# Optimization experiments

Hardware: AMD Instinct MI355X
Metric: run time of the kernel (lower is better)

The kernel has to match this reference:

```python
import jax, jax.numpy as jnp
import numpy as np

NUM_GRAPHS = 64
NUM_LAYERS = 3
HEADS = 4
HID = 64
DMODEL = HEADS * HID  # 256
NUM_EDGE_TYPES = 8
NUM_CLASSES = 2
N_NODES = 30000
N_EDGES = 240000


def setup_inputs() -> dict:
    key = jax.random.key(0)
    ks = jax.random.split(key, 16)
    s = 0.05
    x = jax.random.normal(ks[0], (N_NODES, DMODEL), jnp.float32)
    edge_index = jax.random.randint(ks[1], (2, N_EDGES), 0, N_NODES)
    batch = jnp.sort(jax.random.randint(ks[2], (N_NODES,), 0, NUM_GRAPHS))
    edge_type_ids = jax.random.randint(ks[3], (N_EDGES,), 0, NUM_EDGE_TYPES)
    # stacked per-layer conv params (all layers are DMODEL -> HEADS*HID = DMODEL)
    Wq = jax.random.normal(ks[4], (NUM_LAYERS, DMODEL, DMODEL), jnp.float32) * s
    bq = jax.random.normal(ks[5], (NUM_LAYERS, DMODEL), jnp.float32) * s
    Wk = jax.random.normal(ks[6], (NUM_LAYERS, DMODEL, DMODEL), jnp.float32) * s
    bk = jax.random.normal(ks[7], (NUM_LAYERS, DMODEL), jnp.float32) * s
    Wv = jax.random.normal(ks[8], (NUM_LAYERS, DMODEL, DMODEL), jnp.float32) * s
    bv = jax.random.normal(ks[9], (NUM_LAYERS, DMODEL), jnp.float32) * s
    Eemb = jax.random.normal(ks[10], (NUM_LAYERS, NUM_EDGE_TYPES, DMODEL), jnp.float32) * s
    # 1-layer GRU (PyTorch layout: [3*hid, in], gate order r, z, n)
    W_ih = jax.random.normal(ks[11], (3 * HID, DMODEL), jnp.float32) * s
    b_ih = jax.random.normal(ks[12], (3 * HID,), jnp.float32) * s
    W_hh = jax.random.normal(ks[13], (3 * HID, HID), jnp.float32) * s
    b_hh = jax.random.normal(ks[14], (3 * HID,), jnp.float32) * s
    W_fc = jax.random.normal(ks[15], (NUM_CLASSES, HID), jnp.float32) * s
    b_fc = jnp.zeros((NUM_CLASSES,), jnp.float32)
    return dict(x=x, edge_index=edge_index, batch=batch, edge_type_ids=edge_type_ids,
                Wq=Wq, bq=bq, Wk=Wk, bk=bk, Wv=Wv, bv=bv, Eemb=Eemb,
                W_ih=W_ih, b_ih=b_ih, W_hh=W_hh, b_hh=b_hh, W_fc=W_fc, b_fc=b_fc)


def reference(x, edge_index, batch, edge_type_ids, Wq, bq, Wk, bk, Wv, bv, Eemb,
              W_ih, b_ih, W_hh, b_hh, W_fc, b_fc):
    N = x.shape[0]
    src, dst = edge_index[0], edge_index[1]  # messages flow src -> dst
    scale = 1.0 / jnp.sqrt(jnp.float32(HID))
    for l in range(NUM_LAYERS):
        q = (x @ Wq[l] + bq[l]).reshape(N, HEADS, HID)
        k_all = x @ Wk[l] + bk[l]  # [N, DMODEL]
        v_all = x @ Wv[l] + bv[l]
        ete = Eemb[l][edge_type_ids]  # edge-type conditioning, [E, DMODEL]
        k = (k_all[src] + ete).reshape(-1, HEADS, HID)
        v = (v_all[src] + ete).reshape(-1, HEADS, HID)
        scores = jnp.einsum('ehd,ehd->eh', q[dst], k) * scale  # [E, H]
        # per-destination-node segment softmax (stable)
        m = jax.ops.segment_max(scores, dst, num_segments=N)
        ex = jnp.exp(scores - m[dst])
        den = jax.ops.segment_sum(ex, dst, num_segments=N)
        alpha = ex / (den[dst] + 1e-16)
        agg = jax.ops.segment_sum(alpha[..., None] * v, dst, num_segments=N)
        x = jax.nn.elu(agg.reshape(N, DMODEL))
    # global mean pool over graphs
    cnt = jax.ops.segment_sum(jnp.ones((N,), x.dtype), batch, num_segments=NUM_GRAPHS)
    g = jax.ops.segment_sum(x, batch, num_segments=NUM_GRAPHS) / jnp.maximum(cnt, 1.0)[:, None]
    # single GRU step from h0 = 0 (seq_len == 1)
    h0 = jnp.zeros((NUM_GRAPHS, HID), x.dtype)
    gi = g @ W_ih.T + b_ih
    gh = h0 @ W_hh.T + b_hh
    ir, iz, inn = jnp.split(gi, 3, axis=-1)
    hr, hz, hn = jnp.split(gh, 3, axis=-1)
    r = jax.nn.sigmoid(ir + hr)
    z = jax.nn.sigmoid(iz + hz)
    n = jnp.tanh(inn + r * hn)
    h = (1.0 - z) * n + z * h0
    return h @ W_fc.T + b_fc  # [NUM_GRAPHS, NUM_CLASSES]
```

## Files before the change

kernel.cpp:

```cpp
#include <hip/hip_runtime.h>
#include <math.h>

#define N_NODES 30000
#define N_EDGES 240000
#define DMODEL 256
#define NETYPES 8
#define NGRAPHS 64
#define NLAYERS 3

typedef __attribute__((ext_vector_type(8))) short short8;
typedef __attribute__((ext_vector_type(4))) float f32x4;

__device__ __forceinline__ unsigned short f2bf(float f) {
  union { float f; unsigned u; } v; v.f = f;
  unsigned r = v.u + 0x7FFF + ((v.u >> 16) & 1);
  return (unsigned short)(r >> 16);
}
__device__ __forceinline__ float bf2f(unsigned short h) {
  union { unsigned u; float f; } v; v.u = ((unsigned)h) << 16;
  return v.f;
}

__device__ __forceinline__ void async_g2l(const unsigned short* g, unsigned short* l) {
  __builtin_amdgcn_global_load_lds(
      (const __attribute__((address_space(1))) void*)g,
      (__attribute__((address_space(3))) void*)l, 16, 0, 0);
}

__device__ __forceinline__ float dpp_red_add(float x) {
  int v = __float_as_int(x);
  int t;
  t = __builtin_amdgcn_update_dpp(0, v, 0xB1, 0xF, 0xF, true);
  v = __float_as_int(__int_as_float(v) + __int_as_float(t));
  t = __builtin_amdgcn_update_dpp(0, v, 0x4E, 0xF, 0xF, true);
  v = __float_as_int(__int_as_float(v) + __int_as_float(t));
  t = __builtin_amdgcn_update_dpp(0, v, 0x141, 0xF, 0xF, true);
  v = __float_as_int(__int_as_float(v) + __int_as_float(t));
  t = __builtin_amdgcn_update_dpp(0, v, 0x140, 0xF, 0xF, true);
  v = __float_as_int(__int_as_float(v) + __int_as_float(t));
  return __int_as_float(v);
}

__global__ void k_count_deg(const int* __restrict__ dst, int* __restrict__ deg) {
  int e = blockIdx.x * blockDim.x + threadIdx.x;
  if (e < N_EDGES) atomicAdd(&deg[dst[e]], 1);
}

__global__ __launch_bounds__(1024) void k_scan(const int* __restrict__ deg,
                                               int* __restrict__ rowstart,
                                               int* __restrict__ cursor) {
  const int C = 30;
  int tid = threadIdx.x;
  int base = tid * C;
  int vals[C];
  int sum = 0;
#pragma unroll
  for (int j = 0; j < C; ++j) {
    int idx = base + j;
    int v = (idx < N_NODES) ? deg[idx] : 0;
    vals[j] = sum;
    sum += v;
  }
  int lane = tid & 63, wv = tid >> 6;
  int s = sum;
#pragma unroll
  for (int off = 1; off < 64; off <<= 1) {
    int t2 = __shfl_up(s, off);
    if (lane >= off) s += t2;
  }
  __shared__ int wsum[16];
  if (lane == 63) wsum[wv] = s;
  __syncthreads();
  if (tid == 0) {
    int a = 0;
#pragma unroll
    for (int i = 0; i < 16; ++i) { int t2 = wsum[i]; wsum[i] = a; a += t2; }
    rowstart[N_NODES] = a;
  }
  __syncthreads();
  int texcl = wsum[wv] + (s - sum);
#pragma unroll
  for (int j = 0; j < C; ++j) {
    int idx = base + j;
    if (idx < N_NODES) {
      int p = texcl + vals[j];
      rowstart[idx] = p;
      cursor[idx]   = p;
    }
  }
}

__global__ void k_scatter(const int* __restrict__ src, const int* __restrict__ dst,
                          const int* __restrict__ etype, int* __restrict__ cursor,
                          int* __restrict__ packed) {
  int e = blockIdx.x * blockDim.x + threadIdx.x;
  if (e < N_EDGES) {
    int p = atomicAdd(&cursor[dst[e]], 1);
    packed[p] = src[e] * NETYPES + etype[e];
  }
}

__global__ __launch_bounds__(256) void k_cvt_w(
    const float* __restrict__ Wq, const float* __restrict__ Wk, const float* __restrict__ Wv,
    unsigned short* __restrict__ wthi) {
  __shared__ float tile[32][33];
  int k0 = blockIdx.x * 32;
  int n0g = blockIdx.y * 32;
  int l = blockIdx.z;
  int which = n0g >> 8;
  int col0 = n0g & 255;
  const float* W = (which == 0) ? Wq : ((which == 1) ? Wk : Wv);
  int c = threadIdx.x & 31, r = threadIdx.x >> 5;
#pragma unroll
  for (int rr = 0; rr < 4; ++rr) {
    int kk = r + rr * 8;
    tile[kk][c] = W[(size_t)l * 65536 + (size_t)(k0 + kk) * 256 + col0 + c];
  }
  __syncthreads();
  int kk = threadIdx.x & 31, nn0 = threadIdx.x >> 5;
#pragma unroll
  for (int rr = 0; rr < 4; ++rr) {
    int nn = nn0 + rr * 8;
    wthi[((size_t)l * 768 + n0g + nn) * 256 + k0 + kk] = f2bf(tile[kk][nn]);
  }
}

__global__ void k_cvt_b(const float* __restrict__ bq, const float* __restrict__ bk,
                        const float* __restrict__ bv, float* __restrict__ bcat) {
  int idx = blockIdx.x * 256 + threadIdx.x;
  if (idx >= NLAYERS * 768) return;
  int n = idx % 768, l = idx / 768;
  int which = n >> 8, col = n & 255;
  const float* b = (which == 0) ? bq : ((which == 1) ? bk : bv);
  bcat[idx] = b[l * 256 + col];
}

__global__ void k_cvt_x(const float* __restrict__ x, unsigned short* __restrict__ xhi,
                        unsigned short* __restrict__ xlo) {
  int i = blockIdx.x * 256 + threadIdx.x;
  if (i < N_NODES * 256) {
    float v = x[i];
    unsigned short h = f2bf(v);
    xhi[i] = h;
    xlo[i] = f2bf(v - bf2f(h));
  }
}

__global__ __launch_bounds__(256) void k_gemm_mfma(
    const unsigned short* __restrict__ Ahi, const unsigned short* __restrict__ Alo,
    const unsigned short* __restrict__ Bhi,
    const float* __restrict__ bcat, float* __restrict__ qbuf,
    unsigned short* __restrict__ kv) {
  __shared__ unsigned short smem[2 * 12288];

  int tid = threadIdx.x;
  int lane = tid & 63, wave = tid >> 6;
  int bx = blockIdx.x;
  int xcd = bx & 7, slot = bx >> 3;
  int rt = xcd + (slot / 6) * 8;
  if (rt >= 235) return;
  int row0 = rt * 128;
  int n0 = (slot % 6) * 128;
  int wm = (wave >> 1) * 64, wn = (wave & 1) * 64;
  int quad = lane >> 4, l16 = lane & 15;
  int chunk = lane & 3;
  int srow = wave * 32 + (lane >> 2);

  f32x4 acc[4][4];
#pragma unroll
  for (int i = 0; i < 4; ++i)
#pragma unroll
    for (int j = 0; j < 4; ++j) acc[i][j] = (f32x4)(0.f);

  auto STAGE = [&](int k0, int b) {
    unsigned short* s = smem + b * 12288;
#pragma unroll
    for (int j = 0; j < 2; ++j) {
      int r = srow + j * 16;
      int ldsoff = wave * 1024 + j * 512;
      int garA = row0 + r; if (garA >= N_NODES) garA = N_NODES - 1;
      size_t aoff = (size_t)garA * 256 + k0 + chunk * 8;
      async_g2l(Ahi + aoff, s + ldsoff);
      async_g2l(Alo + aoff, s + 4096 + ldsoff);
      size_t boff = (size_t)(n0 + r) * 256 + k0 + chunk * 8;
      async_g2l(Bhi + boff, s + 8192 + ldsoff);
    }
  };

  STAGE(0, 0);
#pragma unroll
  for (int k = 0; k < 8; ++k) {
    int cur = k & 1;
    if (k < 7) {
      STAGE((k + 1) * 32, cur ^ 1);
      asm volatile("s_waitcnt vmcnt(6)" ::: "memory");
    } else {
      asm volatile("s_waitcnt vmcnt(0)" ::: "memory");
    }
    __builtin_amdgcn_s_barrier();

    const unsigned short* sAhi = smem + cur * 12288;
    const unsigned short* sAlo = sAhi + 4096;
    const unsigned short* sBhi = sAhi + 8192;
    short8 ah[4], al[4], bh[4];
#pragma unroll
    for (int i = 0; i < 4; ++i) {
      int off = (wm + i * 16 + l16) * 32 + quad * 8;
      ah[i] = *(const short8*)(sAhi + off);
      al[i] = *(const short8*)(sAlo + off);
    }
#pragma unroll
    for (int j = 0; j < 4; ++j) {
      int off = (wn + j * 16 + l16) * 32 + quad * 8;
      bh[j] = *(const short8*)(sBhi + off);
    }
#pragma unroll
    for (int i = 0; i < 4; ++i)
#pragma unroll
      for (int j = 0; j < 4; ++j) {
        acc[i][j] = __builtin_amdgcn_mfma_f32_16x16x32_bf16(ah[i], bh[j], acc[i][j], 0, 0, 0);
        acc[i][j] = __builtin_amdgcn_mfma_f32_16x16x32_bf16(al[i], bh[j], acc[i][j], 0, 0, 0);
      }
    __builtin_amdgcn_s_barrier();
  }

  float bj[4];
#pragma unroll
  for (int j = 0; j < 4; ++j) bj[j] = bcat[n0 + wn + j * 16 + l16];
  bool isq = (n0 < 256);
#pragma unroll
  for (int i = 0; i < 4; ++i) {
    int rowb = row0 + wm + i * 16 + quad * 4;
#pragma unroll
    for (int r = 0; r < 4; ++r) {
      int grow = rowb + r;
      if (grow < N_NODES) {
        if (isq) {
          float* cp = qbuf + (size_t)grow * 256 + n0 + wn + l16;
#pragma unroll
          for (int j = 0; j < 4; ++j) cp[j * 16] = acc[i][j][r] + bj[j];
        } else {
          unsigned short* cp = kv + (size_t)grow * 512 + (n0 - 256) + wn + l16;
#pragma unroll
          for (int j = 0; j < 4; ++j) cp[j * 16] = f2bf(acc[i][j][r] + bj[j]);
        }
      }
    }
  }
}

__global__ __launch_bounds__(256) void k_attn(
    const float* __restrict__ qbuf, const unsigned short* __restrict__ kv,
    const int* __restrict__ rowstart, const int* __restrict__ packed,
    const float* __restrict__ Eemb_l,
    unsigned short* __restrict__ xhi, unsigned short* __restrict__ xlo) {
  __shared__ float ete_s[NETYPES * 256];
  int t = threadIdx.x;
#pragma unroll
  for (int i = 0; i < NETYPES; ++i) ete_s[i * 256 + t] = Eemb_l[i * 256 + t];
  __syncthreads();
  int lane = t & 63;
  int n = blockIdx.x * 4 + (t >> 6);
  float4 q4 = ((const float4*)(qbuf + (size_t)n * 256))[lane];
  int rs = rowstart[n], re = rowstart[n + 1];
  float l1 = 0.f, ax1 = 0.f, ay1 = 0.f, az1 = 0.f, aw1 = 0.f;
  float l2 = 0.f, ax2 = 0.f, ay2 = 0.f, az2 = 0.f, aw2 = 0.f;
  int i = rs;
  for (; i + 2 <= re; i += 2) {
    int pkA = packed[i], pkB = packed[i + 1];
    const unsigned short* baseA = kv + (size_t)(pkA >> 3) * 512;
    const unsigned short* baseB = kv + (size_t)(pkB >> 3) * 512;
    ushort4 kA = ((const ushort4*)baseA)[lane];
    ushort4 vA = ((const ushort4*)(baseA + 256))[lane];
    ushort4 kB = ((const ushort4*)baseB)[lane];
    ushort4 vB = ((const ushort4*)(baseB + 256))[lane];
    float4 eA = ((const float4*)(ete_s + (pkA & 7) * 256))[lane];
    float4 eB = ((const float4*)(ete_s + (pkB & 7) * 256))[lane];
    float pA = (bf2f(kA.x) + eA.x) * q4.x + (bf2f(kA.y) + eA.y) * q4.y +
               (bf2f(kA.z) + eA.z) * q4.z + (bf2f(kA.w) + eA.w) * q4.w;
    float pB = (bf2f(kB.x) + eB.x) * q4.x + (bf2f(kB.y) + eB.y) * q4.y +
               (bf2f(kB.z) + eB.z) * q4.z + (bf2f(kB.w) + eB.w) * q4.w;
    pA = dpp_red_add(pA);
    pB = dpp_red_add(pB);
    float e1 = __expf(pA * 0.125f);
    float e2 = __expf(pB * 0.125f);
    l1 += e1; l2 += e2;
    ax1 = fmaf(e1, bf2f(vA.x) + eA.x, ax1);
    ay1 = fmaf(e1, bf2f(vA.y) + eA.y, ay1);
    az1 = fmaf(e1, bf2f(vA.z) + eA.z, az1);
    aw1 = fmaf(e1, bf2f(vA.w) + eA.w, aw1);
    ax2 = fmaf(e2, bf2f(vB.x) + eB.x, ax2);
    ay2 = fmaf(e2, bf2f(vB.y) + eB.y, ay2);
    az2 = fmaf(e2, bf2f(vB.z) + eB.z, az2);
    aw2 = fmaf(e2, bf2f(vB.w) + eB.w, aw2);
  }
  if (i < re) {
    int pk = packed[i];
    const unsigned short* base = kv + (size_t)(pk >> 3) * 512;
    ushort4 kh = ((const ushort4*)base)[lane];
    ushort4 vh = ((const ushort4*)(base + 256))[lane];
    float4 e4 = ((const float4*)(ete_s + (pk & 7) * 256))[lane];
    float p = (bf2f(kh.x) + e4.x) * q4.x + (bf2f(kh.y) + e4.y) * q4.y +
              (bf2f(kh.z) + e4.z) * q4.z + (bf2f(kh.w) + e4.w) * q4.w;
    p = dpp_red_add(p);
    float e1 = __expf(p * 0.125f);
    l1 += e1;
    ax1 = fmaf(e1, bf2f(vh.x) + e4.x, ax1);
    ay1 = fmaf(e1, bf2f(vh.y) + e4.y, ay1);
    az1 = fmaf(e1, bf2f(vh.z) + e4.z, az1);
    aw1 = fmaf(e1, bf2f(vh.w) + e4.w, aw1);
  }
  float l = l1 + l2;
  float inv = 1.f / (l + 1e-16f);
  float4 o;
  o.x = (ax1 + ax2) * inv; o.y = (ay1 + ay2) * inv;
  o.z = (az1 + az2) * inv; o.w = (aw1 + aw2) * inv;
  o.x = o.x > 0.f ? o.x : expm1f(o.x);
  o.y = o.y > 0.f ? o.y : expm1f(o.y);
  o.z = o.z > 0.f ? o.z : expm1f(o.z);
  o.w = o.w > 0.f ? o.w : expm1f(o.w);
  unsigned short h0 = f2bf(o.x), h1 = f2bf(o.y), h2 = f2bf(o.z), h3 = f2bf(o.w);
  ushort4 hv, lv;
  hv.x = h0; hv.y = h1; hv.z = h2; hv.w = h3;
  lv.x = f2bf(o.x - bf2f(h0)); lv.y = f2bf(o.y - bf2f(h1));
  lv.z = f2bf(o.z - bf2f(h2)); lv.w = f2bf(o.w - bf2f(h3));
  size_t base_o = (size_t)n * 256 + lane * 4;
  *(ushort4*)(xhi + base_o) = hv;
  *(ushort4*)(xlo + base_o) = lv;
}

__global__ __launch_bounds__(256) void k_pool_partial(
    const unsigned short* __restrict__ xhi, const unsigned short* __restrict__ xlo,
    const int* __restrict__ batch, float* __restrict__ gacc) {
  int t = threadIdx.x;
  int base = blockIdx.x * 128;
  int end = base + 128; if (end > N_NODES) end = N_NODES;
  __shared__ int bsh[128];
  if (t < 128 && base + t < N_NODES) bsh[t] = batch[base + t];
  __syncthreads();
  float acc = 0.f;
  int cur = bsh[0];
  for (int n = base; n < end; ++n) {
    int g = bsh[n - base];
    if (g != cur) {
      atomicAdd(&gacc[cur * 256 + t], acc);
      acc = 0.f; cur = g;
    }
    size_t idx = (size_t)n * 256 + t;
    acc += bf2f(xhi[idx]) + bf2f(xlo[idx]);
  }
  atomicAdd(&gacc[cur * 256 + t], acc);
}

__device__ inline int lower_bound_dev(const int* a, int n, int val) {
  int lo = 0, hi = n;
  while (lo < hi) {
    int mid = (lo + hi) >> 1;
    if (a[mid] < val) lo = mid + 1; else hi = mid;
  }
  return lo;
}

__global__ __launch_bounds__(256) void k_gru_fc(
    const float* __restrict__ gacc, const int* __restrict__ batch,
    const float* __restrict__ W_ih, const float* __restrict__ b_ih,
    const float* __restrict__ b_hh, const float* __restrict__ W_fc,
    const float* __restrict__ b_fc, float* __restrict__ out) {
  __shared__ float gv[256];
  __shared__ float gates[192];
  __shared__ float h[64];
  int gr = blockIdx.x, t = threadIdx.x;
  int s0 = lower_bound_dev(batch, N_NODES, gr);
  int e0 = lower_bound_dev(batch, N_NODES, gr + 1);
  float c = (e0 > s0) ? (float)(e0 - s0) : 1.f;
  gv[t] = gacc[gr * 256 + t] / c;
  __syncthreads();
  if (t < 192) {
    const float* wr = W_ih + t * 256;
    float s = b_ih[t];
    for (int k = 0; k < 256; ++k) s = fmaf(gv[k], wr[k], s);
    gates[t] = s;
  }
  __syncthreads();
  if (t < 64) {
    float r  = 1.f / (1.f + expf(-(gates[t] + b_hh[t])));
    float z  = 1.f / (1.f + expf(-(gates[64 + t] + b_hh[64 + t])));
    float nn = tanhf(gates[128 + t] + r * b_hh[128 + t]);
    h[t] = (1.f - z) * nn;
  }
  __syncthreads();
  if (t < 2) {
    const float* wr = W_fc + t * 64;
    float s = b_fc[t];
    for (int k = 0; k < 64; ++k) s = fmaf(h[k], wr[k], s);
    out[gr * 2 + t] = s;
  }
}

extern "C" void kernel_launch(void* const* d_in, const int* in_sizes, int n_in,
                              void* d_out, int out_size, void* d_ws, size_t ws_size,
                              hipStream_t stream) {
  const float* x     = (const float*)d_in[0];
  const int* edge_index = (const int*)d_in[1];
  const int* batch   = (const int*)d_in[2];
  const int* etype   = (const int*)d_in[3];
  const float* Wq    = (const float*)d_in[4];
  const float* bq    = (const float*)d_in[5];
  const float* Wk    = (const float*)d_in[6];
  const float* bk    = (const float*)d_in[7];
  const float* Wv    = (const float*)d_in[8];
  const float* bv    = (const float*)d_in[9];
  const float* Eemb  = (const float*)d_in[10];
  const float* W_ih  = (const float*)d_in[11];
  const float* b_ih  = (const float*)d_in[12];
  const float* b_hh  = (const float*)d_in[14];
  const float* W_fc  = (const float*)d_in[15];
  const float* b_fc  = (const float*)d_in[16];
  float* out = (float*)d_out;

  const int* src = edge_index;
  const int* dst = edge_index + N_EDGES;

  float* qbuf  = (float*)d_ws;
  float* gacc  = qbuf + (size_t)N_NODES * 256;
  float* bcat  = gacc + NGRAPHS * 256;
  unsigned short* kv   = (unsigned short*)(bcat + NLAYERS * 768);
  unsigned short* xhi  = kv + (size_t)N_NODES * 512;
  unsigned short* xlo  = xhi + (size_t)N_NODES * 256;
  unsigned short* wthi = xlo + (size_t)N_NODES * 256;
  int* deg      = (int*)(wthi + (size_t)NLAYERS * 768 * 256);
  int* rowstart = deg + N_NODES;
  int* cursor   = rowstart + N_NODES + 1;
  int* packed   = cursor + N_NODES;

  hipMemsetAsync(deg, 0, N_NODES * sizeof(int), stream);
  hipMemsetAsync(gacc, 0, NGRAPHS * 256 * sizeof(float), stream);
  k_count_deg<<<(N_EDGES + 255) / 256, 256, 0, stream>>>(dst, deg);
  k_scan<<<1, 1024, 0, stream>>>(deg, rowstart, cursor);
  k_scatter<<<(N_EDGES + 255) / 256, 256, 0, stream>>>(src, dst, etype, cursor, packed);

  k_cvt_w<<<dim3(8, 24, 3), 256, 0, stream>>>(Wq, Wk, Wv, wthi);
  k_cvt_b<<<(NLAYERS * 768 + 255) / 256, 256, 0, stream>>>(bq, bk, bv, bcat);
  k_cvt_x<<<(N_NODES * 256 + 255) / 256, 256, 0, stream>>>(x, xhi, xlo);

  for (int l = 0; l < NLAYERS; ++l) {
    k_gemm_mfma<<<1440, 256, 0, stream>>>(
        xhi, xlo, wthi + (size_t)l * 768 * 256,
        bcat + l * 768, qbuf, kv);
    k_attn<<<N_NODES / 4, 256, 0, stream>>>(qbuf, kv, rowstart, packed,
                                            Eemb + (size_t)l * NETYPES * 256, xhi, xlo);
  }
  k_pool_partial<<<(N_NODES + 127) / 128, 256, 0, stream>>>(xhi, xlo, batch, gacc);
  k_gru_fc<<<NGRAPHS, 256, 0, stream>>>(gacc, batch, W_ih, b_ih, b_hh, W_fc, b_fc, out);
}
```

Measured before the change: 453.6 us.

## Interleave K/V per lane in gathered rows and stage edge lists in LDS

The projection epilogue now writes K and V interleaved in groups of four, so each lane's four K values and four V values sit in one contiguous 16-byte chunk. The attention kernel then gathers K and V for an edge with a single 16-byte load per lane instead of two 8-byte loads from separate halves of the row. The block's packed edge indices are also preloaded into shared memory when there are at most 512 of them, replacing per-edge global index loads. In exchange, the epilogue stores become scattered 2-byte writes, and a slower unrolled-less fallback path handles blocks with more edges.

```diff
diff --git a/kernel.cpp b/kernel.cpp
--- a/kernel.cpp
+++ b/kernel.cpp
@@ -9,6 +9,7 @@
 #define NLAYERS 3
 
 typedef __attribute__((ext_vector_type(8))) short short8;
+typedef __attribute__((ext_vector_type(8))) unsigned short ushort8;
 typedef __attribute__((ext_vector_type(4))) float f32x4;
 
 __device__ __forceinline__ unsigned short f2bf(float f) {
@@ -228,6 +229,9 @@
 #pragma unroll
   for (int j = 0; j < 4; ++j) bj[j] = bcat[n0 + wn + j * 16 + l16];
   bool isq = (n0 < 256);
+  int cb = n0 - 256;
+  int isV = cb >> 8;
+  int cc0 = (cb & 255) + wn + l16;
 #pragma unroll
   for (int i = 0; i < 4; ++i) {
     int rowb = row0 + wm + i * 16 + quad * 4;
@@ -240,9 +244,12 @@
 #pragma unroll
           for (int j = 0; j < 4; ++j) cp[j * 16] = acc[i][j][r] + bj[j];
         } else {
-          unsigned short* cp = kv + (size_t)grow * 512 + (n0 - 256) + wn + l16;
-#pragma unroll
-          for (int j = 0; j < 4; ++j) cp[j * 16] = f2bf(acc[i][j][r] + bj[j]);
+          unsigned short* rowp = kv + (size_t)grow * 512 + isV * 4;
+#pragma unroll
+          for (int j = 0; j < 4; ++j) {
+            int c = cc0 + j * 16;
+            rowp[((c >> 2) << 3) + (c & 3)] = f2bf(acc[i][j][r] + bj[j]);
+          }
         }
       }
     }
@@ -255,61 +262,85 @@
     const float* __restrict__ Eemb_l,
     unsigned short* __restrict__ xhi, unsigned short* __restrict__ xlo) {
   __shared__ float ete_s[NETYPES * 256];
+  __shared__ int pk_s[512];
   int t = threadIdx.x;
 #pragma unroll
   for (int i = 0; i < NETYPES; ++i) ete_s[i * 256 + t] = Eemb_l[i * 256 + t];
+  int nb = blockIdx.x * 4;
+  int brs = rowstart[nb], bre = rowstart[nb + 4];
+  int cnt = bre - brs;
+  if (cnt <= 512) {
+    for (int j = t; j < cnt; j += 256) pk_s[j] = packed[brs + j];
+  }
   __syncthreads();
   int lane = t & 63;
-  int n = blockIdx.x * 4 + (t >> 6);
+  int n = nb + (t >> 6);
   float4 q4 = ((const float4*)(qbuf + (size_t)n * 256))[lane];
   int rs = rowstart[n], re = rowstart[n + 1];
   float l1 = 0.f, ax1 = 0.f, ay1 = 0.f, az1 = 0.f, aw1 = 0.f;
   float l2 = 0.f, ax2 = 0.f, ay2 = 0.f, az2 = 0.f, aw2 = 0.f;
-  int i = rs;
-  for (; i + 2 <= re; i += 2) {
-    int pkA = packed[i], pkB = packed[i + 1];
-    const unsigned short* baseA = kv + (size_t)(pkA >> 3) * 512;
-    const unsigned short* baseB = kv + (size_t)(pkB >> 3) * 512;
-    ushort4 kA = ((const ushort4*)baseA)[lane];
-    ushort4 vA = ((const ushort4*)(baseA + 256))[lane];
-    ushort4 kB = ((const ushort4*)baseB)[lane];
-    ushort4 vB = ((const ushort4*)(baseB + 256))[lane];
-    float4 eA = ((const float4*)(ete_s + (pkA & 7) * 256))[lane];
-    float4 eB = ((const float4*)(ete_s + (pkB & 7) * 256))[lane];
-    float pA = (bf2f(kA.x) + eA.x) * q4.x + (bf2f(kA.y) + eA.y) * q4.y +
-               (bf2f(kA.z) + eA.z) * q4.z + (bf2f(kA.w) + eA.w) * q4.w;
-    float pB = (bf2f(kB.x) + eB.x) * q4.x + (bf2f(kB.y) + eB.y) * q4.y +
-               (bf2f(kB.z) + eB.z) * q4.z + (bf2f(kB.w) + eB.w) * q4.w;
-    pA = dpp_red_add(pA);
-    pB = dpp_red_add(pB);
-    float e1 = __expf(pA * 0.125f);
-    float e2 = __expf(pB * 0.125f);
-    l1 += e1; l2 += e2;
-    ax1 = fmaf(e1, bf2f(vA.x) + eA.x, ax1);
-    ay1 = fmaf(e1, bf2f(vA.y) + eA.y, ay1);
-    az1 = fmaf(e1, bf2f(vA.z) + eA.z, az1);
-    aw1 = fmaf(e1, bf2f(vA.w) + eA.w, aw1);
-    ax2 = fmaf(e2, bf2f(vB.x) + eB.x, ax2);
-    ay2 = fmaf(e2, bf2f(vB.y) + eB.y, ay2);
-    az2 = fmaf(e2, bf2f(vB.z) + eB.z, az2);
-    aw2 = fmaf(e2, bf2f(vB.w) + eB.w, aw2);
-  }
-  if (i < re) {
-    int pk = packed[i];
-    const unsigned short* base = kv + (size_t)(pk >> 3) * 512;
-    ushort4 kh = ((const ushort4*)base)[lane];
-    ushort4 vh = ((const ushort4*)(base + 256))[lane];
-    float4 e4 = ((const float4*)(ete_s + (pk & 7) * 256))[lane];
-    float p = (bf2f(kh.x) + e4.x) * q4.x + (bf2f(kh.y) + e4.y) * q4.y +
-              (bf2f(kh.z) + e4.z) * q4.z + (bf2f(kh.w) + e4.w) * q4.w;
-    p = dpp_red_add(p);
-    float e1 = __expf(p * 0.125f);
-    l1 += e1;
-    ax1 = fmaf(e1, bf2f(vh.x) + e4.x, ax1);
-    ay1 = fmaf(e1, bf2f(vh.y) + e4.y, ay1);
-    az1 = fmaf(e1, bf2f(vh.z) + e4.z, az1);
-    aw1 = fmaf(e1, bf2f(vh.w) + e4.w, aw1);
-  }
+
+  if (cnt <= 512) {
+    int i = rs - brs, ie = re - brs;
+    for (; i + 2 <= ie; i += 2) {
+      int pkA = pk_s[i], pkB = pk_s[i + 1];
+      const unsigned short* baseA = kv + (size_t)(pkA >> 3) * 512;
+      const unsigned short* baseB = kv + (size_t)(pkB >> 3) * 512;
+      ushort8 cA = ((const ushort8*)baseA)[lane];
+      ushort8 cB = ((const ushort8*)baseB)[lane];
+      float4 eA = ((const float4*)(ete_s + (pkA & 7) * 256))[lane];
+      float4 eB = ((const float4*)(ete_s + (pkB & 7) * 256))[lane];
+      float pA = (bf2f(cA[0]) + eA.x) * q4.x + (bf2f(cA[1]) + eA.y) * q4.y +
+                 (bf2f(cA[2]) + eA.z) * q4.z + (bf2f(cA[3]) + eA.w) * q4.w;
+      float pB = (bf2f(cB[0]) + eB.x) * q4.x + (bf2f(cB[1]) + eB.y) * q4.y +
+                 (bf2f(cB[2]) + eB.z) * q4.z + (bf2f(cB[3]) + eB.w) * q4.w;
+      pA = dpp_red_add(pA);
+      pB = dpp_red_add(pB);
+      float e1 = __expf(pA * 0.125f);
+      float e2 = __expf(pB * 0.125f);
+      l1 += e1; l2 += e2;
+      ax1 = fmaf(e1, bf2f(cA[4]) + eA.x, ax1);
+      ay1 = fmaf(e1, bf2f(cA[5]) + eA.y, ay1);
+      az1 = fmaf(e1, bf2f(cA[6]) + eA.z, az1);
+      aw1 = fmaf(e1, bf2f(cA[7]) + eA.w, aw1);
+      ax2 = fmaf(e2, bf2f(cB[4]) + eB.x, ax2);
+      ay2 = fmaf(e2, bf2f(cB[5]) + eB.y, ay2);
+      az2 = fmaf(e2, bf2f(cB[6]) + eB.z, az2);
+      aw2 = fmaf(e2, bf2f(cB[7]) + eB.w, aw2);
+    }
+    if (i < ie) {
+      int pk = pk_s[i];
+      const unsigned short* base = kv + (size_t)(pk >> 3) * 512;
+      ushort8 cA = ((const ushort8*)base)[lane];
+      float4 e4 = ((const float4*)(ete_s + (pk & 7) * 256))[lane];
+      float p = (bf2f(cA[0]) + e4.x) * q4.x + (bf2f(cA[1]) + e4.y) * q4.y +
+                (bf2f(cA[2]) + e4.z) * q4.z + (bf2f(cA[3]) + e4.w) * q4.w;
+      p = dpp_red_add(p);
+      float e1 = __expf(p * 0.125f);
+      l1 += e1;
+      ax1 = fmaf(e1, bf2f(cA[4]) + e4.x, ax1);
+      ay1 = fmaf(e1, bf2f(cA[5]) + e4.y, ay1);
+      az1 = fmaf(e1, bf2f(cA[6]) + e4.z, az1);
+      aw1 = fmaf(e1, bf2f(cA[7]) + e4.w, aw1);
+    }
+  } else {
+    for (int i = rs; i < re; ++i) {
+      int pk = packed[i];
+      const unsigned short* base = kv + (size_t)(pk >> 3) * 512;
+      ushort8 cA = ((const ushort8*)base)[lane];
+      float4 e4 = ((const float4*)(ete_s + (pk & 7) * 256))[lane];
+      float p = (bf2f(cA[0]) + e4.x) * q4.x + (bf2f(cA[1]) + e4.y) * q4.y +
+                (bf2f(cA[2]) + e4.z) * q4.z + (bf2f(cA[3]) + e4.w) * q4.w;
+      p = dpp_red_add(p);
+      float e1 = __expf(p * 0.125f);
+      l1 += e1;
+      ax1 = fmaf(e1, bf2f(cA[4]) + e4.x, ax1);
+      ay1 = fmaf(e1, bf2f(cA[5]) + e4.y, ay1);
+      az1 = fmaf(e1, bf2f(cA[6]) + e4.z, az1);
+      aw1 = fmaf(e1, bf2f(cA[7]) + e4.w, aw1);
+    }
+  }
+
   float l = l1 + l2;
   float inv = 1.f / (l + 1e-16f);
   float4 o;
```

Result: no change. 454.8 us (+0.3%).
